# Optimization experiments

Hardware: AMD Instinct MI355X
Metric: run time of the kernel (lower is better)

Reference implementation:

```python
import jax, jax.numpy as jnp
from jax import lax
import numpy as np

L = 1024   # latent_size
R = 128    # latent_size // k
G = 2      # groups
KS = 2     # kernel_size
BI, BT, T, TXT = 32, 128, 64, 300
EPS = 1e-5


def setup_inputs() -> dict:
    key = jax.random.key(0)
    ks = jax.random.split(key, 24)
    n = lambda i, shape, s=0.05: jax.random.normal(ks[i], shape, jnp.float32) * s
    return {
        "img_embed": jax.random.normal(ks[0], (BI, 36, L), jnp.float32),
        "cap_embed": jax.random.normal(ks[1], (BT, T, TXT), jnp.float32),
        # reduce_img / reduce_txt (1x1 conv == linear over channels)
        "W_ri": n(2, (R, L)), "b_ri": n(3, (R,)),
        "W_rt": n(4, (R, TXT)), "b_rt": n(5, (R,)),
        # two MixedConv blocks stacked on a leading axis of size 2
        "mk_W": n(6, (2, R * R * KS // G, R)), "mk_b": n(7, (2, R * R * KS // G)),  # hypernet kernel Linear
        "mbias_W": n(8, (2, R, R)), "mbias_b": n(9, (2, R)),                        # hypernet bias Linear
        "wn_g": 1.0 + n(10, (2, R), 0.1), "wn_b": n(11, (2, R), 0.1),               # BN over generated kernel
        "ca_W": n(12, (2, R, R // G, KS)), "ca_b": n(13, (2, R)),                   # static grouped conv1a
        "bn_g": 1.0 + n(14, (2, 2 * R), 0.1), "bn_b": n(15, (2, 2 * R), 0.1),       # BN on cat activations
        "c1_W": n(16, (2, R, 2 * R)), "c1_b": n(17, (2, R)),                        # 1x1 mixing conv
        # txt_fc 1x1 conv
        "W_fc": n(18, (L, R)), "b_fc": n(19, (L,)),
    }


def _bn(x, g, b):
    # training-mode BatchNorm1d over (N, C, L): stats per channel over (N, L)
    m = x.mean(axis=(0, 2), keepdims=True)
    v = x.var(axis=(0, 2), keepdims=True)
    return g[None, :, None] * (x - m) * lax.rsqrt(v + EPS) + b[None, :, None]


def _gconv(x, w):
    # grouped valid conv1d, x: (B, Cin, T), w: (Cout, Cin//G, KS)
    return lax.conv_general_dilated(x, w, (1,), 'VALID',
                                    feature_group_count=G,
                                    dimension_numbers=('NCH', 'OIH', 'NCH'))


def _l2norm(x, axis=-1):
    return x / jnp.linalg.norm(x, axis=axis, keepdims=True)


def reference(img_embed, cap_embed, W_ri, b_ri, W_rt, b_rt, mk_W, mk_b,
              mbias_W, mbias_b, wn_g, wn_b, ca_W, ca_b, bn_g, bn_b,
              c1_W, c1_b, W_fc, b_fc):
    imgs = img_embed.transpose(0, 2, 1)   # (BI, L, 36)
    caps = cap_embed.transpose(0, 2, 1)   # (BT, 300, T)
    img_global = imgs.mean(-1)            # (BI, L)
    cap_red = jnp.einsum('oc,bct->bot', W_rt, caps) + b_rt[None, :, None]  # (BT, R, T)
    img_red = jnp.einsum('oc,bct->bot', W_ri, imgs) + b_ri[None, :, None]  # (BI, R, 36)
    img_vec = img_red.mean(-1)            # (BI, R) hypernet conditioning

    def mixed(x, base, j):
        # hypernet-generated grouped conv kernel + bias
        kern = (mk_W[j] @ base + mk_b[j]).reshape(R, R // G, KS)  # (out, in//g, ks)
        kern = _bn(kern.transpose(1, 0, 2), wn_g[j], wn_b[j]).transpose(1, 0, 2)
        bias = mbias_W[j] @ base + mbias_b[j]                     # (R,)
        px = _gconv(x, kern) + bias[None, :, None]
        ax = _gconv(x, ca_W[j]) + ca_b[j][None, :, None]
        h = jnp.concatenate([px, ax], axis=1)                     # (BT, 2R, T')
        h = jax.nn.relu(_bn(h, bn_g[j], bn_b[j]))
        return jnp.einsum('oc,bct->bot', c1_W[j], h) + c1_b[j][None, :, None]

    def per_image(base, img_g):
        x = mixed(cap_red, base, 0)
        x = mixed(x, base, 1)
        x = jnp.einsum('oc,bct->bot', W_fc, x) + b_fc[None, :, None]  # (BT, L, T-2)
        tv = _l2norm(jnp.max(x, axis=-1), axis=-1)                    # (BT, L)
        iv = _l2norm(img_g, axis=-1)                                  # (L,)
        return tv @ iv                                                # (BT,)

    sims = jax.vmap(per_image)(img_vec, img_global)  # (BI, BT)
    return sims
```

## Files before the change

kernel.cpp:

```cpp
#include <hip/hip_runtime.h>


#define EPSc 1e-5f
typedef unsigned short u16;
typedef __bf16 bf16x8 __attribute__((ext_vector_type(8)));
typedef float f32x4 __attribute__((ext_vector_type(4)));

static const long OFF_IMG_GLOBAL = 0;
static const long OFF_IV         = 32768;
static const long OFF_IMG_VEC    = 65536;
static const long OFF_CAP_RED    = 69632;
static const long OFF_KERN       = 1118208;
static const long OFF_KERN_BF    = 2166784;
static const long OFF_CA_BF      = 2691072;
static const long OFF_C1W0       = 2707456;
static const long OFF_C1W1       = 2715648;
static const long OFF_WFC        = 2732032;
static const long OFF_CAP_BF     = 2797568;
static const long OFF_SHARED1    = 3330112;
static const long OFF_ST_AX0     = 4378688;
static const long FIXED_END      = 4378944;

__device__ inline u16 f2bf(float f) {
  union { float f; unsigned u; } v; v.f = f;
  unsigned u = v.u;
  return (u16)((u + 0x7FFFu + ((u >> 16) & 1u)) >> 16);
}
__device__ inline float bf2f(u16 u) {
  union { unsigned u; float f; } v; v.u = ((unsigned)u) << 16; return v.f;
}

__global__ void k_img(const float* __restrict__ img, float* __restrict__ img_global,
                      float* __restrict__ iv) {
  int b = blockIdx.x, tid = threadIdx.x;
  __shared__ float gl[1024];
  __shared__ float red[256];
  float ssq = 0.f;
  for (int l = tid; l < 1024; l += 256) {
    float s = 0.f;
    for (int p = 0; p < 36; ++p) s += img[((long)b*36 + p)*1024 + l];
    float g = s * (1.f/36.f);
    gl[l] = g;
    img_global[(long)b*1024 + l] = g;
    ssq += g*g;
  }
  red[tid] = ssq;
  __syncthreads();
  for (int off = 128; off > 0; off >>= 1) {
    if (tid < off) red[tid] += red[tid+off];
    __syncthreads();
  }
  float inv = rsqrtf(red[0]);
  for (int l = tid; l < 1024; l += 256) iv[(long)b*1024 + l] = gl[l]*inv;
}

__global__ void k_imgvec(const float* __restrict__ img_global, const float* __restrict__ W_ri,
                         const float* __restrict__ b_ri, float* __restrict__ img_vec) {
  int b = blockIdx.x, tid = threadIdx.x;
  __shared__ float gl[1024];
  for (int l = tid; l < 1024; l += 128) gl[l] = img_global[(long)b*1024 + l];
  __syncthreads();
  const float* w = W_ri + (long)tid*1024;
  float acc = b_ri[tid];
  for (int l = 0; l < 1024; l += 4) {
    float4 wv = *(const float4*)(w + l);
    float4 gv = *(const float4*)(gl + l);
    acc += wv.x*gv.x + wv.y*gv.y + wv.z*gv.z + wv.w*gv.w;
  }
  img_vec[(long)b*128 + tid] = acc;
}

__global__ void k_capred(const float* __restrict__ cap, const float* __restrict__ W_rt,
                         const float* __restrict__ b_rt, float* __restrict__ cap_red) {
  int tg = blockIdx.x, b = blockIdx.y, tid = threadIdx.x;
  __shared__ float xs[300*16];
  for (int idx = tid; idx < 16*300; idx += 128) {
    int q = idx / 300, c = idx - q*300;
    xs[c*16 + q] = cap[((long)b*64 + tg*16 + q)*300 + c];
  }
  __syncthreads();
  int o = tid;
  const float* w = W_rt + (long)o*300;
  float acc[16];
  float bb = b_rt[o];
  #pragma unroll
  for (int q = 0; q < 16; ++q) acc[q] = bb;
  for (int c = 0; c < 300; ++c) {
    float wv = w[c];
    const float* xp = &xs[c*16];
    float4 x0 = *(const float4*)(xp);
    float4 x1 = *(const float4*)(xp+4);
    float4 x2 = *(const float4*)(xp+8);
    float4 x3 = *(const float4*)(xp+12);
    acc[0]+=wv*x0.x; acc[1]+=wv*x0.y; acc[2]+=wv*x0.z; acc[3]+=wv*x0.w;
    acc[4]+=wv*x1.x; acc[5]+=wv*x1.y; acc[6]+=wv*x1.z; acc[7]+=wv*x1.w;
    acc[8]+=wv*x2.x; acc[9]+=wv*x2.y; acc[10]+=wv*x2.z; acc[11]+=wv*x2.w;
    acc[12]+=wv*x3.x; acc[13]+=wv*x3.y; acc[14]+=wv*x3.z; acc[15]+=wv*x3.w;
  }
  float* outp = cap_red + ((long)b*128 + o)*64 + tg*16;
  #pragma unroll
  for (int q = 0; q < 16; ++q) outp[q] = acc[q];
}

__global__ void k_cap2bf(const float* __restrict__ cap_red, u16* __restrict__ cap_bf) {
  int b = blockIdx.x, tid = threadIdx.x;
  __shared__ float ls[128*64];
  for (int idx = tid; idx < 8192; idx += 256) ls[idx] = cap_red[(long)b*8192 + idx];
  __syncthreads();
  for (int idx = tid; idx < 65*128; idx += 256) {
    int t = idx >> 7, c = idx & 127;
    float v = (t < 64) ? ls[c*64 + t] : 0.f;
    cap_bf[((long)b*65 + t)*128 + c] = f2bf(v);
  }
}

__global__ void k_kerngen(const float* __restrict__ mk_W, const float* __restrict__ mk_b,
                          const float* __restrict__ img_vec, float* __restrict__ kern) {
  int j = blockIdx.x >> 7, kb = blockIdx.x & 127, tid = threadIdx.x;
  int k = kb*128 + tid;
  __shared__ float bl[128*32];
  for (int idx = tid; idx < 4096; idx += 128) {
    int i = idx >> 7, r = idx & 127;
    bl[r*32 + i] = img_vec[idx];
  }
  __syncthreads();
  const float* wrow = mk_W + ((long)j*16384 + k)*128;
  float acc[32];
  #pragma unroll
  for (int i = 0; i < 32; ++i) acc[i] = 0.f;
  for (int r = 0; r < 128; ++r) {
    float w = wrow[r];
    const float* bp = &bl[r*32];
    #pragma unroll
    for (int i = 0; i < 32; ++i) acc[i] += w * bp[i];
  }
  float kb_ = mk_b[(long)j*16384 + k];
  for (int i = 0; i < 32; ++i)
    kern[((long)j*32 + i)*16384 + k] = acc[i] + kb_;
}

__global__ void k_kernbn(const float* __restrict__ kern, const float* __restrict__ wn_g,
                         const float* __restrict__ wn_b, u16* __restrict__ kbf) {
  int j = blockIdx.x >> 5, i = blockIdx.x & 31, o = threadIdx.x;
  const float* row = kern + ((long)((j*32+i)*128 + o))*128;
  float s = 0.f, q = 0.f;
  for (int c = 0; c < 128; ++c) { float v = row[c]; s += v; q += v*v; }
  float mean = s * (1.f/128.f);
  float var = q * (1.f/128.f) - mean*mean;
  float rstd = rsqrtf(var + EPSc);
  float sc = wn_g[j*128+o] * rstd;
  float sh = wn_b[j*128+o] - mean*sc;
  int g = o >> 6, op = o & 63;
  u16* base = kbf + (((long)(j*32+i)*2 + g)*2)*4096 + op*64;
  for (int c = 0; c < 128; ++c) {
    float v = row[c]*sc + sh;
    int kp = c & 1, cp = c >> 1;
    base[(long)kp*4096 + cp] = f2bf(v);
  }
}

__global__ void k_ca2bf(const float* __restrict__ caW, u16* __restrict__ cabf) {
  int idx = blockIdx.x*256 + threadIdx.x;
  int j = idx >> 14, r = idx & 16383;
  int o = r >> 7, ck = r & 127, cp = ck >> 1, kp = ck & 1;
  int g = o >> 6, op = o & 63;
  cabf[(((long)(j*2+g)*2 + kp))*4096 + op*64 + cp] = f2bf(caW[idx]);
}

__global__ void k_c1bf(const float* __restrict__ c1W, u16* __restrict__ w0, u16* __restrict__ w1) {
  int idx = blockIdx.x*256 + threadIdx.x;
  if (idx < 16384) { int o = idx >> 7, c = idx & 127; w0[idx] = f2bf(c1W[o*256 + c]); }
  else { int e = idx - 16384; w1[e] = f2bf(c1W[32768 + e]); }
}

__global__ void k_wfc2bf(const float* __restrict__ W, u16* __restrict__ out) {
  int idx = (blockIdx.x*256 + threadIdx.x)*4;
  float4 v = *(const float4*)(W + idx);
  u16 o[4] = { f2bf(v.x), f2bf(v.y), f2bf(v.z), f2bf(v.w) };
  *(uint2*)(out + idx) = *(const uint2*)(o);
}

__global__ void k_conv(const float* __restrict__ X, long xstr, int Tin, int Tout,
                       const float* __restrict__ Wt, long wstr,
                       const float* __restrict__ bias, int bstr,
                       float* __restrict__ Y, long ystr) {
  int b = blockIdx.x, ic = blockIdx.y, tid = threadIdx.x;
  __shared__ float xls[128*64];
  const float* Xb = X + (long)ic*xstr + (long)b*128*Tin;
  for (int idx = tid; idx < 128*Tin; idx += 256) {
    int c = idx / Tin, t = idx - c*Tin;
    xls[c*64 + t] = Xb[idx];
  }
  __syncthreads();
  int oi = tid & 63, tq = tid >> 6;
  int o0 = oi*2, g = o0 >> 6, t0 = tq*16;
  const float* wa = Wt + (long)ic*wstr + (long)o0*128;
  const float* wb = wa + 128;
  float acc0[16], acc1[16];
  #pragma unroll
  for (int tt = 0; tt < 16; ++tt) { acc0[tt] = 0.f; acc1[tt] = 0.f; }
  bool f16ok = (t0 + 16 < Tin);
  for (int cp = 0; cp < 64; ++cp) {
    float wa0 = wa[cp*2], wa1 = wa[cp*2+1];
    float wb0 = wb[cp*2], wb1 = wb[cp*2+1];
    const float* row = &xls[(g*64 + cp)*64 + t0];
    float f[17];
    float4 v0 = *(const float4*)(row);
    float4 v1 = *(const float4*)(row+4);
    float4 v2 = *(const float4*)(row+8);
    float4 v3 = *(const float4*)(row+12);
    f[0]=v0.x; f[1]=v0.y; f[2]=v0.z; f[3]=v0.w;
    f[4]=v1.x; f[5]=v1.y; f[6]=v1.z; f[7]=v1.w;
    f[8]=v2.x; f[9]=v2.y; f[10]=v2.z; f[11]=v2.w;
    f[12]=v3.x; f[13]=v3.y; f[14]=v3.z; f[15]=v3.w;
    f[16] = f16ok ? row[16] : 0.f;
    #pragma unroll
    for (int tt = 0; tt < 16; ++tt) {
      acc0[tt] += wa0*f[tt] + wa1*f[tt+1];
      acc1[tt] += wb0*f[tt] + wb1*f[tt+1];
    }
  }
  float bb0 = bias[ic*bstr + o0], bb1 = bias[ic*bstr + o0 + 1];
  float* y0 = Y + (long)ic*ystr + ((long)b*128 + o0)*Tout;
  float* y1 = y0 + Tout;
  #pragma unroll
  for (int tt = 0; tt < 16; ++tt) {
    int t = t0 + tt;
    if (t < Tout) { y0[t] = acc0[tt] + bb0; y1[t] = acc1[tt] + bb1; }
  }
}

__global__ void k_stats(const float* __restrict__ X, long xstr, int Tlen,
                        const float* __restrict__ gp, const float* __restrict__ bp,
                        float* __restrict__ st, int sstr) {
  int c = blockIdx.x, ic = blockIdx.y, tid = threadIdx.x;
  __shared__ float r1[256], r2[256];
  const float* base = X + (long)ic*xstr + (long)c*Tlen;
  int n = 128*Tlen;
  float s = 0.f, q = 0.f;
  for (int idx = tid; idx < n; idx += 256) {
    int b = idx / Tlen, t = idx - b*Tlen;
    float v = base[(long)b*128*Tlen + t];
    s += v; q += v*v;
  }
  r1[tid] = s; r2[tid] = q;
  __syncthreads();
  for (int off = 128; off > 0; off >>= 1) {
    if (tid < off) { r1[tid] += r1[tid+off]; r2[tid] += r2[tid+off]; }
    __syncthreads();
  }
  if (tid == 0) {
    float mean = r1[0] / n;
    float var = r2[0] / n - mean*mean;
    float rstd = rsqrtf(var + EPSc);
    float sc = gp[c]*rstd;
    st[(long)ic*sstr + c] = sc;
    st[(long)ic*sstr + 128 + c] = bp[c] - mean*sc;
  }
}

__global__ void k_mix_shared(const float* __restrict__ X1, const float* __restrict__ st,
                             const float* __restrict__ W, float* __restrict__ Y) {
  int b = blockIdx.x, tid = threadIdx.x;
  __shared__ float xs[128*64];
  __shared__ float ssc[128], ssh[128];
  int o4 = (tid & 31)*4, t0 = (tid >> 5)*8;
  float acc[4][8];
  #pragma unroll
  for (int r = 0; r < 4; ++r)
    #pragma unroll
    for (int tt = 0; tt < 8; ++tt) acc[r][tt] = 0.f;
  if (tid < 128) { ssc[tid] = st[tid]; ssh[tid] = st[128+tid]; }
  __syncthreads();
  const float* Xb = X1 + (long)b*128*63;
  for (int idx = tid; idx < 128*63; idx += 256) {
    int c = idx / 63, t = idx - c*63;
    xs[c*64 + t] = fmaxf(Xb[idx]*ssc[c] + ssh[c], 0.f);
  }
  __syncthreads();
  for (int c = 0; c < 128; ++c) {
    float4 f0 = *(const float4*)&xs[c*64 + t0];
    float4 f1 = *(const float4*)&xs[c*64 + t0 + 4];
    #pragma unroll
    for (int r = 0; r < 4; ++r) {
      float w = W[(long)(o4+r)*256 + 128 + c];
      acc[r][0] += w*f0.x; acc[r][1] += w*f0.y; acc[r][2] += w*f0.z; acc[r][3] += w*f0.w;
      acc[r][4] += w*f1.x; acc[r][5] += w*f1.y; acc[r][6] += w*f1.z; acc[r][7] += w*f1.w;
    }
  }
  #pragma unroll
  for (int r = 0; r < 4; ++r)
    #pragma unroll
    for (int tt = 0; tt < 8; ++tt) {
      int t = t0 + tt;
      if (t < 63) Y[((long)b*64 + t)*128 + o4 + r] = acc[r][tt];
    }
}

__global__ __launch_bounds__(256) void k_conv_mfma2(
    const u16* __restrict__ X, long x_img_str, int tr_stride,
    const u16* __restrict__ kernA, const u16* __restrict__ statA,
    int tvalid, u16* __restrict__ H, int ctot, float* __restrict__ part) {
  int bc = blockIdx.x, v = blockIdx.y, i = blockIdx.z;
  int tid = threadIdx.x, w = tid >> 6, lane = tid & 63;
  int l15 = lane & 15, l4 = lane >> 4;
  int g = v & 1;
  const u16* A = (v >= 2) ? (statA + (long)g*8192)
                          : (kernA + (long)i*16384 + (long)g*8192);
  __shared__ u16 xls[65*64];
  bf16x8 af[2][2];
  #pragma unroll
  for (int kp = 0; kp < 2; ++kp)
    #pragma unroll
    for (int ks = 0; ks < 2; ++ks)
      af[kp][ks] = *(const bf16x8*)(A + ((long)(kp*64 + w*16 + l15))*64 + ks*32 + l4*8);
  int cbase = v*64 + w*16;
  float s[4] = {0.f,0.f,0.f,0.f}, q[4] = {0.f,0.f,0.f,0.f};
  for (int bb = 0; bb < 8; ++bb) {
    int b = bc*8 + bb;
    const u16* src = X + x_img_str*i + ((long)b*tr_stride)*128 + g*64;
    __syncthreads();
    for (int idx = tid; idx < 65*8; idx += 256) {
      int r = idx >> 3, ch = idx & 7;
      uint4 d = *(const uint4*)(src + (long)r*128 + ch*8);
      *(uint4*)(xls + r*64 + ((ch ^ (r & 7))*8)) = d;
    }
    __syncthreads();
    #pragma unroll
    for (int nt = 0; nt < 4; ++nt) {
      f32x4 acc = {0.f,0.f,0.f,0.f};
      #pragma unroll
      for (int kp = 0; kp < 2; ++kp) {
        int row = nt*16 + l15 + kp;
        #pragma unroll
        for (int ks = 0; ks < 2; ++ks) {
          int ch = (ks*4 + l4) ^ (row & 7);
          bf16x8 bf = *(const bf16x8*)(xls + row*64 + ch*8);
          acc = __builtin_amdgcn_mfma_f32_16x16x32_bf16(af[kp][ks], bf, acc, 0, 0, 0);
        }
      }
      int t = nt*16 + l15;
      u16 h4[4] = { f2bf(acc[0]), f2bf(acc[1]), f2bf(acc[2]), f2bf(acc[3]) };
      *(uint2*)(H + ((long)((i*128 + b)*64 + t))*ctot + cbase + l4*4) = *(const uint2*)(h4);
      float m = (t < tvalid) ? 1.f : 0.f;
      #pragma unroll
      for (int r = 0; r < 4; ++r) {
        float vv = acc[r]*m;
        s[r] += vv; q[r] += vv*vv;
      }
    }
  }
  #pragma unroll
  for (int r = 0; r < 4; ++r) {
    #pragma unroll
    for (int mk = 1; mk < 16; mk <<= 1) {
      s[r] += __shfl_xor(s[r], mk);
      q[r] += __shfl_xor(q[r], mk);
    }
  }
  if (l15 == 0) {
    #pragma unroll
    for (int r = 0; r < 4; ++r) {
      int c = cbase + l4*4 + r;
      long base = ((long)i*ctot + c)*32;
      part[base + bc] = s[r];
      part[base + 16 + bc] = q[r];
    }
  }
}

__global__ void k_finstats2(const float* __restrict__ part, float* __restrict__ scsh,
                            const float* __restrict__ g, const float* __restrict__ bta,
                            int ct, float n, int total) {
  int idx = blockIdx.x*256 + threadIdx.x;
  if (idx >= total) return;
  int c = idx & (ct - 1);
  const float* p = part + (long)idx*32;
  float s = 0.f, q = 0.f;
  #pragma unroll
  for (int k = 0; k < 16; ++k) { s += p[k]; q += p[16+k]; }
  float mean = s / n, var = q / n - mean*mean;
  float sc = g[c] * rsqrtf(var + EPSc);
  scsh[idx*2] = sc;
  scsh[idx*2 + 1] = bta[c] - mean*sc;
}

template<int CK>
__global__ __launch_bounds__(256) void k_mix_mfma2(
    const u16* __restrict__ X, const u16* __restrict__ A,
    const float* __restrict__ scsh,
    const float* __restrict__ c1b, const float* __restrict__ addbuf,
    u16* __restrict__ Q, int tvalid) {
  constexpr int NCH = CK/8;
  constexpr int KST = CK/32;
  int bc = blockIdx.x, m = blockIdx.y, i = blockIdx.z;
  int tid = threadIdx.x, w = tid >> 6, lane = tid & 63;
  int l15 = lane & 15, l4 = lane >> 4;
  __shared__ u16 xls[64*CK];
  __shared__ float lsc[CK], lsh[CK];
  for (int c = tid; c < CK; c += 256) {
    lsc[c] = scsh[((long)i*CK + c)*2];
    lsh[c] = scsh[((long)i*CK + c)*2 + 1];
  }
  int oa = m*64 + w*16 + l15;
  bf16x8 af[KST];
  #pragma unroll
  for (int ks = 0; ks < KST; ++ks)
    af[ks] = *(const bf16x8*)(A + (long)oa*CK + ks*32 + l4*8);
  int ob = m*64 + w*16 + l4*4;
  float4 cb;
  cb.x = c1b[ob]; cb.y = c1b[ob+1]; cb.z = c1b[ob+2]; cb.w = c1b[ob+3];
  for (int bb = 0; bb < 4; ++bb) {
    int b = bc*4 + bb;
    const u16* src = X + ((long)(i*128 + b)*64)*CK;
    __syncthreads();
    for (int idx = tid; idx < 64*NCH; idx += 256) {
      int r = idx / NCH, ch = idx & (NCH - 1);
      uint4 d = *(const uint4*)(src + (long)r*CK + ch*8);
      unsigned dd[4] = {d.x, d.y, d.z, d.w};
      int c0 = ch*8;
      u16 o[8];
      #pragma unroll
      for (int pi = 0; pi < 4; ++pi) {
        float v0 = bf2f((u16)(dd[pi] & 0xFFFF));
        float v1 = bf2f((u16)(dd[pi] >> 16));
        v0 = fmaxf(v0*lsc[c0 + pi*2] + lsh[c0 + pi*2], 0.f);
        v1 = fmaxf(v1*lsc[c0 + pi*2 + 1] + lsh[c0 + pi*2 + 1], 0.f);
        o[pi*2] = f2bf(v0); o[pi*2 + 1] = f2bf(v1);
      }
      *(uint4*)(xls + r*CK + (((ch ^ (r & 15)) & (NCH - 1))*8)) = *(const uint4*)o;
    }
    __syncthreads();
    #pragma unroll
    for (int nt = 0; nt < 4; ++nt) {
      f32x4 acc = {0.f,0.f,0.f,0.f};
      int row = nt*16 + l15;
      #pragma unroll
      for (int ks = 0; ks < KST; ++ks) {
        int ch = ((ks*4 + l4) ^ (row & 15)) & (NCH - 1);
        bf16x8 bf = *(const bf16x8*)(xls + row*CK + ch*8);
        acc = __builtin_amdgcn_mfma_f32_16x16x32_bf16(af[ks], bf, acc, 0, 0, 0);
      }
      int t = row;
      if (t < tvalid) {
        float4 ad = {0.f,0.f,0.f,0.f};
        if (addbuf) ad = *(const float4*)(addbuf + ((long)b*64 + t)*128 + ob);
        u16 h4[4] = { f2bf(acc[0] + cb.x + ad.x), f2bf(acc[1] + cb.y + ad.y),
                      f2bf(acc[2] + cb.z + ad.z), f2bf(acc[3] + cb.w + ad.w) };
        *(uint2*)(Q + ((long)((i*128 + b)*64 + t))*128 + ob) = *(const uint2*)(h4);
      }
    }
  }
}

__global__ __launch_bounds__(256) void k_fc_mfma2(
    const u16* __restrict__ Qt, const u16* __restrict__ Wb,
    const float* __restrict__ bfc, const float* __restrict__ ivp,
    float* __restrict__ outp) {
  int b = blockIdx.x, i = blockIdx.y;
  int tid = threadIdx.x;
  int w = tid >> 6, lane = tid & 63;
  int l15 = lane & 15, l4 = lane >> 4;
  const u16* Qb = Qt + ((long)(i*128 + b))*64*128;
  bf16x8 qf[4][4];
  #pragma unroll
  for (int nt = 0; nt < 4; ++nt)
    #pragma unroll
    for (int ks = 0; ks < 4; ++ks)
      qf[nt][ks] = *(const bf16x8*)(Qb + (nt*16 + l15)*128 + ks*32 + l4*8);
  float ss = 0.f, dd = 0.f;
  const float* ivb = ivp + (long)i*1024;
  float en = (l4 == 0) ? 1.f : 0.f;
  for (int lt = 0; lt < 16; ++lt) {
    int ltg = lt*4 + w;
    const u16* Ab = Wb + (long)(ltg*16 + l15)*128 + l4*8;
    bf16x8 wf0 = *(const bf16x8*)(Ab);
    bf16x8 wf1 = *(const bf16x8*)(Ab + 32);
    bf16x8 wf2 = *(const bf16x8*)(Ab + 64);
    bf16x8 wf3 = *(const bf16x8*)(Ab + 96);
    f32x4 a0 = {0.f,0.f,0.f,0.f}, a1 = {0.f,0.f,0.f,0.f};
    f32x4 a2 = {0.f,0.f,0.f,0.f}, a3 = {0.f,0.f,0.f,0.f};
    a0 = __builtin_amdgcn_mfma_f32_16x16x32_bf16(qf[0][0], wf0, a0, 0,0,0);
    a0 = __builtin_amdgcn_mfma_f32_16x16x32_bf16(qf[0][1], wf1, a0, 0,0,0);
    a0 = __builtin_amdgcn_mfma_f32_16x16x32_bf16(qf[0][2], wf2, a0, 0,0,0);
    a0 = __builtin_amdgcn_mfma_f32_16x16x32_bf16(qf[0][3], wf3, a0, 0,0,0);
    a1 = __builtin_amdgcn_mfma_f32_16x16x32_bf16(qf[1][0], wf0, a1, 0,0,0);
    a1 = __builtin_amdgcn_mfma_f32_16x16x32_bf16(qf[1][1], wf1, a1, 0,0,0);
    a1 = __builtin_amdgcn_mfma_f32_16x16x32_bf16(qf[1][2], wf2, a1, 0,0,0);
    a1 = __builtin_amdgcn_mfma_f32_16x16x32_bf16(qf[1][3], wf3, a1, 0,0,0);
    a2 = __builtin_amdgcn_mfma_f32_16x16x32_bf16(qf[2][0], wf0, a2, 0,0,0);
    a2 = __builtin_amdgcn_mfma_f32_16x16x32_bf16(qf[2][1], wf1, a2, 0,0,0);
    a2 = __builtin_amdgcn_mfma_f32_16x16x32_bf16(qf[2][2], wf2, a2, 0,0,0);
    a2 = __builtin_amdgcn_mfma_f32_16x16x32_bf16(qf[2][3], wf3, a2, 0,0,0);
    a3 = __builtin_amdgcn_mfma_f32_16x16x32_bf16(qf[3][0], wf0, a3, 0,0,0);
    a3 = __builtin_amdgcn_mfma_f32_16x16x32_bf16(qf[3][1], wf1, a3, 0,0,0);
    a3 = __builtin_amdgcn_mfma_f32_16x16x32_bf16(qf[3][2], wf2, a3, 0,0,0);
    a3 = __builtin_amdgcn_mfma_f32_16x16x32_bf16(qf[3][3], wf3, a3, 0,0,0);
    float mx = fmaxf(fmaxf(a0[0], a0[1]), fmaxf(a0[2], a0[3]));
    mx = fmaxf(mx, fmaxf(fmaxf(a1[0], a1[1]), fmaxf(a1[2], a1[3])));
    mx = fmaxf(mx, fmaxf(fmaxf(a2[0], a2[1]), fmaxf(a2[2], a2[3])));
    mx = fmaxf(mx, fmaxf(a3[0], a3[1]));
    if (l4 < 3) mx = fmaxf(mx, fmaxf(a3[2], a3[3]));
    mx = fmaxf(mx, __shfl_xor(mx, 16));
    mx = fmaxf(mx, __shfl_xor(mx, 32));
    int l = ltg*16 + l15;
    float tv = mx + bfc[l];
    ss += en*tv*tv;
    dd += en*tv*ivb[l];
  }
  #pragma unroll
  for (int mk = 1; mk < 64; mk <<= 1) { ss += __shfl_xor(ss, mk); dd += __shfl_xor(dd, mk); }
  __shared__ float s1[4], s2[4];
  if (lane == 0) { s1[w] = ss; s2[w] = dd; }
  __syncthreads();
  if (tid == 0) {
    float S = s1[0]+s1[1]+s1[2]+s1[3];
    float D = s2[0]+s2[1]+s2[2]+s2[3];
    outp[i*128 + b] = D * rsqrtf(S);
  }
}

extern "C" void kernel_launch(void* const* d_in, const int* in_sizes, int n_in,
                              void* d_out, int out_size, void* d_ws, size_t ws_size,
                              hipStream_t stream) {
  (void)in_sizes; (void)n_in; (void)out_size;
  const float* img_embed = (const float*)d_in[0];
  const float* cap_embed = (const float*)d_in[1];
  const float* W_ri  = (const float*)d_in[2];
  const float* b_ri  = (const float*)d_in[3];
  const float* W_rt  = (const float*)d_in[4];
  const float* b_rt  = (const float*)d_in[5];
  const float* mk_W  = (const float*)d_in[6];
  const float* mk_b  = (const float*)d_in[7];
  const float* wn_g  = (const float*)d_in[10];
  const float* wn_b  = (const float*)d_in[11];
  const float* ca_W  = (const float*)d_in[12];
  const float* ca_b  = (const float*)d_in[13];
  const float* bn_g  = (const float*)d_in[14];
  const float* bn_b  = (const float*)d_in[15];
  const float* c1_W  = (const float*)d_in[16];
  const float* c1_b  = (const float*)d_in[17];
  const float* W_fc  = (const float*)d_in[18];
  const float* b_fc  = (const float*)d_in[19];
  float* out = (float*)d_out;
  float* ws  = (float*)d_ws;

  float* img_global = ws + OFF_IMG_GLOBAL;
  float* iv       = ws + OFF_IV;
  float* img_vec  = ws + OFF_IMG_VEC;
  float* cap_red  = ws + OFF_CAP_RED;
  float* kern     = ws + OFF_KERN;
  u16*   kern_bf  = (u16*)(ws + OFF_KERN_BF);
  u16*   ca_bf    = (u16*)(ws + OFF_CA_BF);
  u16*   c1w0     = (u16*)(ws + OFF_C1W0);
  u16*   c1w1     = (u16*)(ws + OFF_C1W1);
  u16*   wfcb     = (u16*)(ws + OFF_WFC);
  u16*   cap_bf   = (u16*)(ws + OFF_CAP_BF);
  float* shared1  = ws + OFF_SHARED1;
  float* st_ax0   = ws + OFF_ST_AX0;

  int NC = 4;
  {
    auto need = [](long nc) -> size_t { return (size_t)(FIXED_END + nc*2621440L + 128) * 4u; };
    if (ws_size >= need(32)) NC = 32;
    else if (ws_size >= need(16)) NC = 16;
    else if (ws_size >= need(8)) NC = 8;
  }

  float* part  = ws + OFF_KERN;
  float* scsh0 = ws + OFF_KERN + 262144;
  float* scsh1 = ws + OFF_KERN + 262144 + 8192;

  long base = FIXED_END;
  float* ax0f = ws + base;
  u16* P0 = (u16*)(ws + base);
  u16* Q0 = (u16*)(ws + base + (long)NC*524288);
  u16* H1 = (u16*)(ws + base + (long)NC*524288*2 + 64);
  u16* Q1 = (u16*)(ws + base + (long)NC*524288*2 + 64 + (long)NC*1048576);

  k_img<<<32, 256, 0, stream>>>(img_embed, img_global, iv);
  k_imgvec<<<32, 128, 0, stream>>>(img_global, W_ri, b_ri, img_vec);
  k_capred<<<dim3(4,128), 128, 0, stream>>>(cap_embed, W_rt, b_rt, cap_red);
  k_cap2bf<<<128, 256, 0, stream>>>(cap_red, cap_bf);
  k_kerngen<<<256, 128, 0, stream>>>(mk_W, mk_b, img_vec, kern);
  k_kernbn<<<64, 128, 0, stream>>>(kern, wn_g, wn_b, kern_bf);
  k_ca2bf<<<128, 256, 0, stream>>>(ca_W, ca_bf);
  k_c1bf<<<192, 256, 0, stream>>>(c1_W, c1w0, c1w1);
  k_wfc2bf<<<128, 256, 0, stream>>>(W_fc, wfcb);

  k_conv<<<dim3(128,1), 256, 0, stream>>>(cap_red, 0, 64, 63, ca_W, 0, ca_b, 0, ax0f, 0);
  k_stats<<<dim3(128,1), 256, 0, stream>>>(ax0f, 0, 63, bn_g+128, bn_b+128, st_ax0, 0);
  k_mix_shared<<<128, 256, 0, stream>>>(ax0f, st_ax0, c1_W, shared1);

  for (int ch = 0; ch < 32/NC; ++ch) {
    int i0 = ch*NC;
    k_conv_mfma2<<<dim3(16,2,NC), 256, 0, stream>>>(
        cap_bf, 0L, 65, kern_bf + (long)i0*16384, ca_bf, 63, P0, 128, part);
    k_finstats2<<<dim3((NC*128+255)/256), 256, 0, stream>>>(
        part, scsh0, bn_g, bn_b, 128, 8064.f, NC*128);
    k_mix_mfma2<128><<<dim3(32,2,NC), 256, 0, stream>>>(
        P0, c1w0, scsh0, c1_b, shared1, Q0, 63);
    k_conv_mfma2<<<dim3(16,4,NC), 256, 0, stream>>>(
        Q0, 1048576L, 64, kern_bf + (long)(32 + i0)*16384, ca_bf + 16384, 62, H1, 256, part);
    k_finstats2<<<dim3((NC*256+255)/256), 256, 0, stream>>>(
        part, scsh1, bn_g + 256, bn_b + 256, 256, 7936.f, NC*256);
    k_mix_mfma2<256><<<dim3(32,2,NC), 256, 0, stream>>>(
        H1, c1w1, scsh1, c1_b + 128, nullptr, Q1, 62);
    k_fc_mfma2<<<dim3(128,NC), 256, 0, stream>>>(
        Q1, wfcb, b_fc, iv + (long)i0*1024, out + i0*128);
  }
}
```

Measured before the change: 655.2 us.

## Keep W_fc fragments in registers across captions and split conv stats grid

The final FC+max kernel now holds a 256-row slice of the bf16 W_fc in registers and loops over 8 captions per block, instead of keeping one caption's activations resident and streaming all of W_fc per block. A small reduction kernel then combines the four slice partials into the cosine similarity. Separately, the conv+stats kernel handles 4 captions per block instead of 8, doubling its grid, with the partial-stat buffers and finstats reduction widened to 32 partials. This is meant to cut redundant weight traffic and raise parallelism, at the cost of an extra launch and more partial-sum memory.

Result: no change. 649.6 us (-0.8%).

```diff
diff --git a/kernel.cpp b/kernel.cpp
--- a/kernel.cpp
+++ b/kernel.cpp
@@ -316,8 +316,8 @@
       af[kp][ks] = *(const bf16x8*)(A + ((long)(kp*64 + w*16 + l15))*64 + ks*32 + l4*8);
   int cbase = v*64 + w*16;
   float s[4] = {0.f,0.f,0.f,0.f}, q[4] = {0.f,0.f,0.f,0.f};
-  for (int bb = 0; bb < 8; ++bb) {
-    int b = bc*8 + bb;
+  for (int bb = 0; bb < 4; ++bb) {
+    int b = bc*4 + bb;
     const u16* src = X + x_img_str*i + ((long)b*tr_stride)*128 + g*64;
     __syncthreads();
     for (int idx = tid; idx < 65*8; idx += 256) {
@@ -362,9 +362,9 @@
     #pragma unroll
     for (int r = 0; r < 4; ++r) {
       int c = cbase + l4*4 + r;
-      long base = ((long)i*ctot + c)*32;
+      long base = ((long)i*ctot + c)*64;
       part[base + bc] = s[r];
-      part[base + 16 + bc] = q[r];
+      part[base + 32 + bc] = q[r];
     }
   }
 }
@@ -375,10 +375,10 @@
   int idx = blockIdx.x*256 + threadIdx.x;
   if (idx >= total) return;
   int c = idx & (ct - 1);
-  const float* p = part + (long)idx*32;
+  const float* p = part + (long)idx*64;
   float s = 0.f, q = 0.f;
   #pragma unroll
-  for (int k = 0; k < 16; ++k) { s += p[k]; q += p[16+k]; }
+  for (int k = 0; k < 32; ++k) { s += p[k]; q += p[32+k]; }
   float mean = s / n, var = q / n - mean*mean;
   float sc = g[c] * rsqrtf(var + EPSc);
   scsh[idx*2] = sc;
@@ -453,71 +453,82 @@
   }
 }
 
-__global__ __launch_bounds__(256) void k_fc_mfma2(
+__global__ __launch_bounds__(256) void k_fc3(
     const u16* __restrict__ Qt, const u16* __restrict__ Wb,
     const float* __restrict__ bfc, const float* __restrict__ ivp,
-    float* __restrict__ outp) {
-  int b = blockIdx.x, i = blockIdx.y;
-  int tid = threadIdx.x;
-  int w = tid >> 6, lane = tid & 63;
+    float* __restrict__ pp) {
+  int bg = blockIdx.x, sl = blockIdx.y, i = blockIdx.z;
+  int tid = threadIdx.x, w = tid >> 6, lane = tid & 63;
   int l15 = lane & 15, l4 = lane >> 4;
-  const u16* Qb = Qt + ((long)(i*128 + b))*64*128;
-  bf16x8 qf[4][4];
-  #pragma unroll
-  for (int nt = 0; nt < 4; ++nt)
+  int lbase = sl*256 + w*64;
+  bf16x8 wf[4][4];
+  #pragma unroll
+  for (int lt = 0; lt < 4; ++lt)
     #pragma unroll
     for (int ks = 0; ks < 4; ++ks)
-      qf[nt][ks] = *(const bf16x8*)(Qb + (nt*16 + l15)*128 + ks*32 + l4*8);
-  float ss = 0.f, dd = 0.f;
+      wf[lt][ks] = *(const bf16x8*)(Wb + (long)(lbase + lt*16 + l15)*128 + ks*32 + l4*8);
+  float bfr[4], ivr[4];
   const float* ivb = ivp + (long)i*1024;
+  #pragma unroll
+  for (int lt = 0; lt < 4; ++lt) {
+    bfr[lt] = bfc[lbase + lt*16 + l15];
+    ivr[lt] = ivb[lbase + lt*16 + l15];
+  }
+  __shared__ float red[4][2];
   float en = (l4 == 0) ? 1.f : 0.f;
-  for (int lt = 0; lt < 16; ++lt) {
-    int ltg = lt*4 + w;
-    const u16* Ab = Wb + (long)(ltg*16 + l15)*128 + l4*8;
-    bf16x8 wf0 = *(const bf16x8*)(Ab);
-    bf16x8 wf1 = *(const bf16x8*)(Ab + 32);
-    bf16x8 wf2 = *(const bf16x8*)(Ab + 64);
-    bf16x8 wf3 = *(const bf16x8*)(Ab + 96);
-    f32x4 a0 = {0.f,0.f,0.f,0.f}, a1 = {0.f,0.f,0.f,0.f};
-    f32x4 a2 = {0.f,0.f,0.f,0.f}, a3 = {0.f,0.f,0.f,0.f};
-    a0 = __builtin_amdgcn_mfma_f32_16x16x32_bf16(qf[0][0], wf0, a0, 0,0,0);
-    a0 = __builtin_amdgcn_mfma_f32_16x16x32_bf16(qf[0][1], wf1, a0, 0,0,0);
-    a0 = __builtin_amdgcn_mfma_f32_16x16x32_bf16(qf[0][2], wf2, a0, 0,0,0);
-    a0 = __builtin_amdgcn_mfma_f32_16x16x32_bf16(qf[0][3], wf3, a0, 0,0,0);
-    a1 = __builtin_amdgcn_mfma_f32_16x16x32_bf16(qf[1][0], wf0, a1, 0,0,0);
-    a1 = __builtin_amdgcn_mfma_f32_16x16x32_bf16(qf[1][1], wf1, a1, 0,0,0);
-    a1 = __builtin_amdgcn_mfma_f32_16x16x32_bf16(qf[1][2], wf2, a1, 0,0,0);
-    a1 = __builtin_amdgcn_mfma_f32_16x16x32_bf16(qf[1][3], wf3, a1, 0,0,0);
-    a2 = __builtin_amdgcn_mfma_f32_16x16x32_bf16(qf[2][0], wf0, a2, 0,0,0);
-    a2 = __builtin_amdgcn_mfma_f32_16x16x32_bf16(qf[2][1], wf1, a2, 0,0,0);
-    a2 = __builtin_amdgcn_mfma_f32_16x16x32_bf16(qf[2][2], wf2, a2, 0,0,0);
-    a2 = __builtin_amdgcn_mfma_f32_16x16x32_bf16(qf[2][3], wf3, a2, 0,0,0);
-    a3 = __builtin_amdgcn_mfma_f32_16x16x32_bf16(qf[3][0], wf0, a3, 0,0,0);
-    a3 = __builtin_amdgcn_mfma_f32_16x16x32_bf16(qf[3][1], wf1, a3, 0,0,0);
-    a3 = __builtin_amdgcn_mfma_f32_16x16x32_bf16(qf[3][2], wf2, a3, 0,0,0);
-    a3 = __builtin_amdgcn_mfma_f32_16x16x32_bf16(qf[3][3], wf3, a3, 0,0,0);
-    float mx = fmaxf(fmaxf(a0[0], a0[1]), fmaxf(a0[2], a0[3]));
-    mx = fmaxf(mx, fmaxf(fmaxf(a1[0], a1[1]), fmaxf(a1[2], a1[3])));
-    mx = fmaxf(mx, fmaxf(fmaxf(a2[0], a2[1]), fmaxf(a2[2], a2[3])));
-    mx = fmaxf(mx, fmaxf(a3[0], a3[1]));
-    if (l4 < 3) mx = fmaxf(mx, fmaxf(a3[2], a3[3]));
-    mx = fmaxf(mx, __shfl_xor(mx, 16));
-    mx = fmaxf(mx, __shfl_xor(mx, 32));
-    int l = ltg*16 + l15;
-    float tv = mx + bfc[l];
-    ss += en*tv*tv;
-    dd += en*tv*ivb[l];
-  }
-  #pragma unroll
-  for (int mk = 1; mk < 64; mk <<= 1) { ss += __shfl_xor(ss, mk); dd += __shfl_xor(dd, mk); }
-  __shared__ float s1[4], s2[4];
-  if (lane == 0) { s1[w] = ss; s2[w] = dd; }
-  __syncthreads();
-  if (tid == 0) {
-    float S = s1[0]+s1[1]+s1[2]+s1[3];
-    float D = s2[0]+s2[1]+s2[2]+s2[3];
-    outp[i*128 + b] = D * rsqrtf(S);
-  }
+  for (int bb = 0; bb < 8; ++bb) {
+    int b = bg*8 + bb;
+    const u16* Qb = Qt + ((long)(i*128 + b))*64*128;
+    float mx[4] = {-3e38f, -3e38f, -3e38f, -3e38f};
+    #pragma unroll
+    for (int nt = 0; nt < 4; ++nt) {
+      bf16x8 qf[4];
+      #pragma unroll
+      for (int ks = 0; ks < 4; ++ks)
+        qf[ks] = *(const bf16x8*)(Qb + (nt*16 + l15)*128 + ks*32 + l4*8);
+      #pragma unroll
+      for (int lt = 0; lt < 4; ++lt) {
+        f32x4 acc = {0.f,0.f,0.f,0.f};
+        acc = __builtin_amdgcn_mfma_f32_16x16x32_bf16(qf[0], wf[lt][0], acc, 0,0,0);
+        acc = __builtin_amdgcn_mfma_f32_16x16x32_bf16(qf[1], wf[lt][1], acc, 0,0,0);
+        acc = __builtin_amdgcn_mfma_f32_16x16x32_bf16(qf[2], wf[lt][2], acc, 0,0,0);
+        acc = __builtin_amdgcn_mfma_f32_16x16x32_bf16(qf[3], wf[lt][3], acc, 0,0,0);
+        float m01 = fmaxf(acc[0], acc[1]);
+        float m23 = fmaxf(acc[2], acc[3]);
+        if (nt == 3 && l4 == 3) m23 = -3e38f;
+        mx[lt] = fmaxf(mx[lt], fmaxf(m01, m23));
+      }
+    }
+    float ssc = 0.f, ddc = 0.f;
+    #pragma unroll
+    for (int lt = 0; lt < 4; ++lt) {
+      float m = mx[lt];
+      m = fmaxf(m, __shfl_xor(m, 16));
+      m = fmaxf(m, __shfl_xor(m, 32));
+      float tv = m + bfr[lt];
+      ssc += en*tv*tv;
+      ddc += en*tv*ivr[lt];
+    }
+    #pragma unroll
+    for (int mk = 1; mk < 16; mk <<= 1) { ssc += __shfl_xor(ssc, mk); ddc += __shfl_xor(ddc, mk); }
+    if (lane == 0) { red[w][0] = ssc; red[w][1] = ddc; }
+    __syncthreads();
+    if (tid == 0) {
+      float S = red[0][0] + red[1][0] + red[2][0] + red[3][0];
+      float D = red[0][1] + red[1][1] + red[2][1] + red[3][1];
+      long o = (((long)i*128 + b)*4 + sl)*2;
+      pp[o] = S; pp[o+1] = D;
+    }
+    __syncthreads();
+  }
+}
+
+__global__ void k_fcred(const float* __restrict__ pp, float* __restrict__ outp) {
+  int i = blockIdx.x, b = threadIdx.x;
+  const float* p = pp + (((long)i*128 + b)*4)*2;
+  float S = p[0] + p[2] + p[4] + p[6];
+  float D = p[1] + p[3] + p[5] + p[7];
+  outp[i*128 + b] = D * rsqrtf(S);
 }
 
 extern "C" void kernel_launch(void* const* d_in, const int* in_sizes, int n_in,
@@ -568,8 +579,9 @@
   }
 
   float* part  = ws + OFF_KERN;
-  float* scsh0 = ws + OFF_KERN + 262144;
-  float* scsh1 = ws + OFF_KERN + 262144 + 8192;
+  float* scsh0 = ws + OFF_KERN + 524288;
+  float* scsh1 = ws + OFF_KERN + 524288 + 8192;
+  float* pp    = ws + OFF_KERN + 524288 + 8192 + 16384;
 
   long base = FIXED_END;
   float* ax0f = ws + base;
@@ -594,19 +606,20 @@
 
   for (int ch = 0; ch < 32/NC; ++ch) {
     int i0 = ch*NC;
-    k_conv_mfma2<<<dim3(16,2,NC), 256, 0, stream>>>(
+    k_conv_mfma2<<<dim3(32,2,NC), 256, 0, stream>>>(
         cap_bf, 0L, 65, kern_bf + (long)i0*16384, ca_bf, 63, P0, 128, part);
     k_finstats2<<<dim3((NC*128+255)/256), 256, 0, stream>>>(
         part, scsh0, bn_g, bn_b, 128, 8064.f, NC*128);
     k_mix_mfma2<128><<<dim3(32,2,NC), 256, 0, stream>>>(
         P0, c1w0, scsh0, c1_b, shared1, Q0, 63);
-    k_conv_mfma2<<<dim3(16,4,NC), 256, 0, stream>>>(
+    k_conv_mfma2<<<dim3(32,4,NC), 256, 0, stream>>>(
         Q0, 1048576L, 64, kern_bf + (long)(32 + i0)*16384, ca_bf + 16384, 62, H1, 256, part);
     k_finstats2<<<dim3((NC*256+255)/256), 256, 0, stream>>>(
         part, scsh1, bn_g + 256, bn_b + 256, 256, 7936.f, NC*256);
     k_mix_mfma2<256><<<dim3(32,2,NC), 256, 0, stream>>>(
         H1, c1w1, scsh1, c1_b + 128, nullptr, Q1, 62);
-    k_fc_mfma2<<<dim3(128,NC), 256, 0, stream>>>(
-        Q1, wfcb, b_fc, iv + (long)i0*1024, out + i0*128);
-  }
-}
+    k_fc3<<<dim3(16,4,NC), 256, 0, stream>>>(
+        Q1, wfcb, b_fc, iv + (long)i0*1024, pp);
+    k_fcred<<<NC, 128, 0, stream>>>(pp, out + i0*128);
+  }
+}
```
